# Kernel tuning notes

Hardware: AMD Instinct MI355X
Metric: run time of the kernel (lower is better)

The kernel has to match this reference:

```python
import jax, jax.numpy as jnp
import numpy as np

B, T, D, H, E = 32, 512, 768, 12, 6  # batch, seq(=input_size), n_embd, num_heads, per-head dim
DFF = 4 * D
EPS = 1e-5


def setup_inputs() -> dict:
    key = jax.random.key(0)
    ks = jax.random.split(key, 10)
    s = 0.02
    return {
        "x": jax.random.normal(ks[0], (B, T, D), jnp.float32),
        "Wq": jax.random.normal(ks[1], (H, D, E), jnp.float32) * s,
        "Wk": jax.random.normal(ks[2], (H, D, E), jnp.float32) * s,
        "Wv": jax.random.normal(ks[3], (H, D, E), jnp.float32) * s,
        "Wo": jax.random.normal(ks[4], (H * E, D), jnp.float32) * s,
        "bo": jnp.zeros((D,), jnp.float32),
        "W1": jax.random.normal(ks[5], (D, DFF), jnp.float32) * s,
        "b1": jnp.zeros((DFF,), jnp.float32),
        "W2": jax.random.normal(ks[6], (DFF, D), jnp.float32) * s,
        "b2": jnp.zeros((D,), jnp.float32),
        "g1": jnp.ones((D,), jnp.float32),
        "beta1": jnp.zeros((D,), jnp.float32),
        "g2": jnp.ones((D,), jnp.float32),
        "beta2": jnp.zeros((D,), jnp.float32),
    }


def _layernorm(x, g, b):
    m = jnp.mean(x, axis=-1, keepdims=True)
    v = jnp.var(x, axis=-1, keepdims=True)  # biased, matches torch LayerNorm
    return (x - m) * jax.lax.rsqrt(v + EPS) * g + b


def reference(x, Wq, Wk, Wv, Wo, bo, W1, b1, W2, b2, g1, beta1, g2, beta2):
    # --- pre-LN multi-head causal attention (dropout = identity, eval mode) ---
    xn = _layernorm(x, g1, beta1)
    q = jnp.einsum("btd,hde->bhte", xn, Wq)
    k = jnp.einsum("btd,hde->bhte", xn, Wk)
    v = jnp.einsum("btd,hde->bhte", xn, Wv)
    scores = jnp.einsum("bhte,bhse->bhts", q, k) * (E ** -0.5)
    causal = jnp.tril(jnp.ones((T, T), dtype=bool))
    scores = jnp.where(causal, scores, -jnp.inf)
    w = jax.nn.softmax(scores, axis=-1)
    o = jnp.einsum("bhts,bhse->bhte", w, v)
    o = o.transpose(0, 2, 1, 3).reshape(B, T, H * E)  # concat heads -> [B,T,72]
    x = x + o @ Wo + bo
    # --- pre-LN feed-forward ---
    y = _layernorm(x, g2, beta2)
    ff = jax.nn.relu(y @ W1 + b1) @ W2 + b2
    return x + ff
```

## Files before the change

kernel.cpp:

```cpp
#include <hip/hip_runtime.h>
#include <hip/hip_bf16.h>

#define BT 16384
#define DIM 768
#define NH 12
#define DFF 3072

typedef __attribute__((ext_vector_type(8))) short short8;
typedef __attribute__((ext_vector_type(4))) float floatx4;

using bf16 = __hip_bfloat16;

static __device__ __forceinline__ float b2f(bf16 v) { return __bfloat162float(v); }
static __device__ __forceinline__ bf16 f2b(float v) { return __float2bfloat16(v); }
static __device__ __forceinline__ void st_o(bf16* p, float v) { *p = __float2bfloat16(v); }
static __device__ __forceinline__ void st_o(float* p, float v) { *p = v; }

static __device__ __forceinline__ void gload_lds16(const void* g, void* l) {
    __builtin_amdgcn_global_load_lds(
        (const __attribute__((address_space(1))) unsigned int*)g,
        (__attribute__((address_space(3))) unsigned int*)l, 16, 0, 0);
}

__global__ __launch_bounds__(256) void pack_small_kernel(
    const float* __restrict__ Wq, const float* __restrict__ Wk, const float* __restrict__ Wv,
    const float* __restrict__ Wo, bf16* __restrict__ wqkv, bf16* __restrict__ wo_t)
{
    int i = blockIdx.x * 256 + threadIdx.x;
    const int S0 = 256 * 768, S1 = 768 * 96;
    if (i < S0) {
        int c = i / 768, dd = i % 768;
        float v = 0.f;
        if (c < 216) {
            int sel = c / 72, cc = c % 72, h = cc / 6, e = cc % 6;
            const float* W = (sel == 0) ? Wq : (sel == 1) ? Wk : Wv;
            v = W[((size_t)h * 768 + dd) * 6 + e];
        }
        wqkv[i] = f2b(v);
    } else if ((i -= S0) < S1) {
        int n = i / 96, r = i % 96;
        wo_t[i] = f2b(r < 72 ? Wo[r * 768 + n] : 0.f);
    }
}

__global__ __launch_bounds__(256) void transpose_kernel(
    const float* __restrict__ in, bf16* __restrict__ out, int R, int C)
{
    __shared__ float t[32][33];
    int c0 = blockIdx.x * 32, r0 = blockIdx.y * 32;
    int cx = threadIdx.x & 31, ry = threadIdx.x >> 5;
#pragma unroll
    for (int j = 0; j < 4; j++)
        t[ry + j * 8][cx] = in[(size_t)(r0 + ry + j * 8) * C + c0 + cx];
    __syncthreads();
    int rx = cx, cy = ry;
#pragma unroll
    for (int j = 0; j < 4; j++)
        out[(size_t)(c0 + cy + j * 8) * R + r0 + rx] = f2b(t[rx][cy + j * 8]);
}

__global__ __launch_bounds__(256) void ln_kernel(
    const float* __restrict__ x, const float* __restrict__ g, const float* __restrict__ be,
    bf16* __restrict__ out)
{
    int row = blockIdx.x;
    int tid = threadIdx.x;
    const float* xr = x + (size_t)row * DIM;
    float v[3], s = 0.f, s2 = 0.f;
#pragma unroll
    for (int i = 0; i < 3; i++) {
        float t = xr[tid + i * 256];
        v[i] = t; s += t; s2 += t * t;
    }
#pragma unroll
    for (int off = 32; off; off >>= 1) {
        s += __shfl_down(s, off);
        s2 += __shfl_down(s2, off);
    }
    __shared__ float red[8];
    int wv = tid >> 6, ln = tid & 63;
    if (ln == 0) { red[wv] = s; red[4 + wv] = s2; }
    __syncthreads();
    float ts = red[0] + red[1] + red[2] + red[3];
    float ts2 = red[4] + red[5] + red[6] + red[7];
    float mean = ts * (1.f / 768.f);
    float var = ts2 * (1.f / 768.f) - mean * mean;
    float rstd = rsqrtf(var + 1e-5f);
    bf16* orow = out + (size_t)row * DIM;
#pragma unroll
    for (int i = 0; i < 3; i++) {
        int dcol = tid + i * 256;
        orow[dcol] = f2b((v[i] - mean) * rstd * g[dcol] + be[dcol]);
    }
}

template <bool RELU, bool BIAS, bool RES, typename OutT>
__global__ __launch_bounds__(256) void gemm_kernel(
    const bf16* __restrict__ A, const bf16* __restrict__ Bt,
    const float* __restrict__ bias, const float* __restrict__ res,
    OutT* __restrict__ C, int M, int N, int K)
{
    __shared__ __align__(16) bf16 lA[128 * 32];
    __shared__ __align__(16) bf16 lB[128 * 32];
    const int tid = threadIdx.x;
    const int bm = blockIdx.x * 128;
    const int bn = blockIdx.y * 128;
    const int wave = tid >> 6, lane = tid & 63;
    const int wm = (wave >> 1) * 64, wn = (wave & 1) * 64;
    const int quad = lane >> 4, l16 = lane & 15;
    const int lrow = lane >> 2;
    const int lkc = (lane & 3) * 8;

    floatx4 acc[4][4] = {};

    for (int k0 = 0; k0 < K; k0 += 32) {
#pragma unroll
        for (int it = 0; it < 2; it++) {
            int r = wave * 32 + it * 16;
            gload_lds16(A + (size_t)(bm + r + lrow) * K + k0 + lkc, lA + r * 32);
            gload_lds16(Bt + (size_t)(bn + r + lrow) * K + k0 + lkc, lB + r * 32);
        }
        __syncthreads();
        short8 af[4], bfr[4];
#pragma unroll
        for (int mt = 0; mt < 4; mt++)
            af[mt] = *(const short8*)(lA + (wm + mt * 16 + l16) * 32 + quad * 8);
#pragma unroll
        for (int nt = 0; nt < 4; nt++)
            bfr[nt] = *(const short8*)(lB + (wn + nt * 16 + l16) * 32 + quad * 8);
#pragma unroll
        for (int mt = 0; mt < 4; mt++)
#pragma unroll
            for (int nt = 0; nt < 4; nt++)
                acc[mt][nt] = __builtin_amdgcn_mfma_f32_16x16x32_bf16(af[mt], bfr[nt], acc[mt][nt], 0, 0, 0);
        __syncthreads();
    }

#pragma unroll
    for (int mt = 0; mt < 4; mt++) {
#pragma unroll
        for (int nt = 0; nt < 4; nt++) {
            int gc = bn + wn + nt * 16 + l16;
            if (gc < N) {
#pragma unroll
                for (int r = 0; r < 4; r++) {
                    int gr = bm + wm + mt * 16 + quad * 4 + r;
                    float v0 = acc[mt][nt][r];
                    if constexpr (BIAS) v0 += bias[gc];
                    if constexpr (RES) v0 += res[(size_t)gr * N + gc];
                    if constexpr (RELU) v0 = fmaxf(v0, 0.f);
                    st_o(C + (size_t)gr * N + gc, v0);
                }
            }
        }
    }
}

__global__ __launch_bounds__(256) void attn_kernel(const bf16* __restrict__ qkv, bf16* __restrict__ o_pad)
{
    int blk = blockIdx.x;
    int half = blk & 1;
    int bh = blk >> 1;
    int b = bh / NH, h = bh % NH;
    int t0 = half * 256;
    int smax = t0 + 256;

    __shared__ float ks[512 * 6];
    __shared__ float vs[512 * 6];
    const bf16* base = qkv + (size_t)b * 512 * 216;
    for (int i = threadIdx.x; i < smax * 6; i += 256) {
        int s = i / 6, e = i % 6;
        ks[i] = b2f(base[s * 216 + 72 + h * 6 + e]);
        vs[i] = b2f(base[s * 216 + 144 + h * 6 + e]);
    }
    __syncthreads();

    int t = t0 + threadIdx.x;
    float q0 = b2f(base[t * 216 + h * 6 + 0]);
    float q1 = b2f(base[t * 216 + h * 6 + 1]);
    float q2 = b2f(base[t * 216 + h * 6 + 2]);
    float q3 = b2f(base[t * 216 + h * 6 + 3]);
    float q4 = b2f(base[t * 216 + h * 6 + 4]);
    float q5 = b2f(base[t * 216 + h * 6 + 5]);

    const float scale = 0.4082482904638630f;
    float m = -1e30f, l = 0.f;
    float o0 = 0, o1 = 0, o2 = 0, o3 = 0, o4 = 0, o5 = 0;
    for (int s = 0; s <= t; s++) {
        const float* kk = &ks[s * 6];
        float sc = (q0 * kk[0] + q1 * kk[1] + q2 * kk[2] + q3 * kk[3] + q4 * kk[4] + q5 * kk[5]) * scale;
        float nm = fmaxf(m, sc);
        float alpha = __expf(m - nm);
        float p = __expf(sc - nm);
        l = l * alpha + p;
        const float* vv = &vs[s * 6];
        o0 = o0 * alpha + p * vv[0];
        o1 = o1 * alpha + p * vv[1];
        o2 = o2 * alpha + p * vv[2];
        o3 = o3 * alpha + p * vv[3];
        o4 = o4 * alpha + p * vv[4];
        o5 = o5 * alpha + p * vv[5];
        m = nm;
    }
    float inv = 1.f / l;
    bf16* orow = o_pad + (size_t)(b * 512 + t) * 96 + h * 6;
    orow[0] = f2b(o0 * inv);
    orow[1] = f2b(o1 * inv);
    orow[2] = f2b(o2 * inv);
    orow[3] = f2b(o3 * inv);
    orow[4] = f2b(o4 * inv);
    orow[5] = f2b(o5 * inv);
}

extern "C" void kernel_launch(void* const* d_in, const int* in_sizes, int n_in,
                              void* d_out, int out_size, void* d_ws, size_t ws_size,
                              hipStream_t stream)
{
    const float* x   = (const float*)d_in[0];
    const float* Wq  = (const float*)d_in[1];
    const float* Wk  = (const float*)d_in[2];
    const float* Wv  = (const float*)d_in[3];
    const float* Wo  = (const float*)d_in[4];
    const float* bo  = (const float*)d_in[5];
    const float* W1  = (const float*)d_in[6];
    const float* b1  = (const float*)d_in[7];
    const float* W2  = (const float*)d_in[8];
    const float* b2  = (const float*)d_in[9];
    const float* g1  = (const float*)d_in[10];
    const float* be1 = (const float*)d_in[11];
    const float* g2  = (const float*)d_in[12];
    const float* be2 = (const float*)d_in[13];

    char* ws = (char*)d_ws;
    size_t off = 0;
    auto alloc = [&](size_t bytes) {
        void* p = ws + off;
        off = (off + bytes + 255) & ~(size_t)255;
        return p;
    };
    bf16*  xn    = (bf16*)alloc((size_t)BT * DIM * 2);
    bf16*  qkvb  = (bf16*)alloc((size_t)BT * 216 * 2);
    bf16*  o_pad = (bf16*)alloc((size_t)BT * 96 * 2);
    float* x1    = (float*)alloc((size_t)BT * DIM * 4);
    bf16*  ffb   = (bf16*)alloc((size_t)BT * DFF * 2);
    bf16*  wqkv  = (bf16*)alloc((size_t)256 * 768 * 2);
    bf16*  wo_t  = (bf16*)alloc((size_t)768 * 96 * 2);
    bf16*  w1t   = (bf16*)alloc((size_t)3072 * 768 * 2);
    bf16*  w2t   = (bf16*)alloc((size_t)768 * 3072 * 2);

    const int PACK_N = 256 * 768 + 768 * 96;
    pack_small_kernel<<<(PACK_N + 255) / 256, 256, 0, stream>>>(Wq, Wk, Wv, Wo, wqkv, wo_t);
    transpose_kernel<<<dim3(3072 / 32, 768 / 32), 256, 0, stream>>>(W1, w1t, 768, 3072);
    transpose_kernel<<<dim3(768 / 32, 3072 / 32), 256, 0, stream>>>(W2, w2t, 3072, 768);

    ln_kernel<<<BT, 256, 0, stream>>>(x, g1, be1, xn);
    gemm_kernel<false, false, false, bf16><<<dim3(128, 2), 256, 0, stream>>>(
        xn, wqkv, nullptr, nullptr, qkvb, BT, 216, 768);
    attn_kernel<<<32 * NH * 2, 256, 0, stream>>>(qkvb, o_pad);
    gemm_kernel<false, true, true, float><<<dim3(128, 6), 256, 0, stream>>>(
        o_pad, wo_t, bo, x, x1, BT, 768, 96);
    ln_kernel<<<BT, 256, 0, stream>>>(x1, g2, be2, xn);
    gemm_kernel<true, true, false, bf16><<<dim3(128, 24), 256, 0, stream>>>(
        xn, w1t, b1, nullptr, ffb, BT, 3072, 768);
    gemm_kernel<false, true, true, float><<<dim3(128, 6), 256, 0, stream>>>(
        ffb, w2t, b2, x1, (float*)d_out, BT, 768, 3072);
}
```

Before: 505.2 us.

## Vectorize layernorm, stage GEMM K in double slabs, LDS-staged bf16 epilogue, balance attention

Layernorm now uses 192 threads, each loading one float4 and writing four packed bf16 values, which cuts per-element memory instructions. The GEMM loads two 32-wide K slabs per barrier pair, halving synchronisations per K step. For bf16 outputs it stages the result tile in LDS and writes it back as coalesced 16-byte stores. Attention blocks now take interleaved 64-row query chunks, so the two halves of each causal head get similar work. The larger LDS footprint may lower GEMM occupancy.

```diff
diff --git a/kernel.cpp b/kernel.cpp
--- a/kernel.cpp
+++ b/kernel.cpp
@@ -8,13 +8,12 @@
 
 typedef __attribute__((ext_vector_type(8))) short short8;
 typedef __attribute__((ext_vector_type(4))) float floatx4;
+typedef __attribute__((ext_vector_type(4))) unsigned short ushort4b;
 
 using bf16 = __hip_bfloat16;
 
 static __device__ __forceinline__ float b2f(bf16 v) { return __bfloat162float(v); }
 static __device__ __forceinline__ bf16 f2b(float v) { return __float2bfloat16(v); }
-static __device__ __forceinline__ void st_o(bf16* p, float v) { *p = __float2bfloat16(v); }
-static __device__ __forceinline__ void st_o(float* p, float v) { *p = v; }
 
 static __device__ __forceinline__ void gload_lds16(const void* g, void* l) {
     __builtin_amdgcn_global_load_lds(
@@ -59,49 +58,53 @@
         out[(size_t)(c0 + cy + j * 8) * R + r0 + rx] = f2b(t[rx][cy + j * 8]);
 }
 
-__global__ __launch_bounds__(256) void ln_kernel(
+__global__ __launch_bounds__(192) void ln_kernel(
     const float* __restrict__ x, const float* __restrict__ g, const float* __restrict__ be,
     bf16* __restrict__ out)
 {
     int row = blockIdx.x;
     int tid = threadIdx.x;
-    const float* xr = x + (size_t)row * DIM;
-    float v[3], s = 0.f, s2 = 0.f;
-#pragma unroll
-    for (int i = 0; i < 3; i++) {
-        float t = xr[tid + i * 256];
-        v[i] = t; s += t; s2 += t * t;
-    }
+    const float4* xr = (const float4*)(x + (size_t)row * DIM);
+    float4 v = xr[tid];
+    float s = v.x + v.y + v.z + v.w;
+    float s2 = v.x * v.x + v.y * v.y + v.z * v.z + v.w * v.w;
 #pragma unroll
     for (int off = 32; off; off >>= 1) {
         s += __shfl_down(s, off);
         s2 += __shfl_down(s2, off);
     }
-    __shared__ float red[8];
+    __shared__ float red[6];
     int wv = tid >> 6, ln = tid & 63;
-    if (ln == 0) { red[wv] = s; red[4 + wv] = s2; }
+    if (ln == 0) { red[wv] = s; red[3 + wv] = s2; }
     __syncthreads();
-    float ts = red[0] + red[1] + red[2] + red[3];
-    float ts2 = red[4] + red[5] + red[6] + red[7];
+    float ts = red[0] + red[1] + red[2];
+    float ts2 = red[3] + red[4] + red[5];
     float mean = ts * (1.f / 768.f);
     float var = ts2 * (1.f / 768.f) - mean * mean;
     float rstd = rsqrtf(var + 1e-5f);
-    bf16* orow = out + (size_t)row * DIM;
-#pragma unroll
-    for (int i = 0; i < 3; i++) {
-        int dcol = tid + i * 256;
-        orow[dcol] = f2b((v[i] - mean) * rstd * g[dcol] + be[dcol]);
-    }
-}
-
-template <bool RELU, bool BIAS, bool RES, typename OutT>
+    int c = tid * 4;
+    float o0 = (v.x - mean) * rstd * g[c + 0] + be[c + 0];
+    float o1 = (v.y - mean) * rstd * g[c + 1] + be[c + 1];
+    float o2 = (v.z - mean) * rstd * g[c + 2] + be[c + 2];
+    float o3 = (v.w - mean) * rstd * g[c + 3] + be[c + 3];
+    bf16 h0 = f2b(o0), h1 = f2b(o1), h2 = f2b(o2), h3 = f2b(o3);
+    ushort4b pk;
+    pk[0] = *(unsigned short*)&h0; pk[1] = *(unsigned short*)&h1;
+    pk[2] = *(unsigned short*)&h2; pk[3] = *(unsigned short*)&h3;
+    *(ushort4b*)(out + (size_t)row * DIM + c) = pk;
+}
+
+template <int NSLAB, bool RELU, bool BIAS, bool RES, bool BF16OUT>
 __global__ __launch_bounds__(256) void gemm_kernel(
     const bf16* __restrict__ A, const bf16* __restrict__ Bt,
     const float* __restrict__ bias, const float* __restrict__ res,
-    OutT* __restrict__ C, int M, int N, int K)
-{
-    __shared__ __align__(16) bf16 lA[128 * 32];
-    __shared__ __align__(16) bf16 lB[128 * 32];
+    void* __restrict__ Cv, int M, int N, int K)
+{
+    constexpr int SMEM_BYTES = BF16OUT ? (128 * 136 * 2) : (NSLAB * 2 * 128 * 32 * 2);
+    __shared__ __align__(16) char smem[SMEM_BYTES];
+    bf16* lA = (bf16*)smem;
+    bf16* lB = lA + NSLAB * 128 * 32;
+
     const int tid = threadIdx.x;
     const int bm = blockIdx.x * 128;
     const int bn = blockIdx.y * 128;
@@ -113,43 +116,82 @@
 
     floatx4 acc[4][4] = {};
 
-    for (int k0 = 0; k0 < K; k0 += 32) {
-#pragma unroll
-        for (int it = 0; it < 2; it++) {
-            int r = wave * 32 + it * 16;
-            gload_lds16(A + (size_t)(bm + r + lrow) * K + k0 + lkc, lA + r * 32);
-            gload_lds16(Bt + (size_t)(bn + r + lrow) * K + k0 + lkc, lB + r * 32);
+    for (int k0 = 0; k0 < K; k0 += NSLAB * 32) {
+#pragma unroll
+        for (int s = 0; s < NSLAB; s++) {
+#pragma unroll
+            for (int it = 0; it < 2; it++) {
+                int r = wave * 32 + it * 16;
+                gload_lds16(A + (size_t)(bm + r + lrow) * K + k0 + s * 32 + lkc,
+                            lA + s * 4096 + r * 32);
+                gload_lds16(Bt + (size_t)(bn + r + lrow) * K + k0 + s * 32 + lkc,
+                            lB + s * 4096 + r * 32);
+            }
         }
         __syncthreads();
-        short8 af[4], bfr[4];
-#pragma unroll
-        for (int mt = 0; mt < 4; mt++)
-            af[mt] = *(const short8*)(lA + (wm + mt * 16 + l16) * 32 + quad * 8);
-#pragma unroll
-        for (int nt = 0; nt < 4; nt++)
-            bfr[nt] = *(const short8*)(lB + (wn + nt * 16 + l16) * 32 + quad * 8);
-#pragma unroll
-        for (int mt = 0; mt < 4; mt++)
+#pragma unroll
+        for (int s = 0; s < NSLAB; s++) {
+            short8 af[4], bfr[4];
+#pragma unroll
+            for (int mt = 0; mt < 4; mt++)
+                af[mt] = *(const short8*)(lA + s * 4096 + (wm + mt * 16 + l16) * 32 + quad * 8);
 #pragma unroll
             for (int nt = 0; nt < 4; nt++)
-                acc[mt][nt] = __builtin_amdgcn_mfma_f32_16x16x32_bf16(af[mt], bfr[nt], acc[mt][nt], 0, 0, 0);
+                bfr[nt] = *(const short8*)(lB + s * 4096 + (wn + nt * 16 + l16) * 32 + quad * 8);
+#pragma unroll
+            for (int mt = 0; mt < 4; mt++)
+#pragma unroll
+                for (int nt = 0; nt < 4; nt++)
+                    acc[mt][nt] = __builtin_amdgcn_mfma_f32_16x16x32_bf16(af[mt], bfr[nt], acc[mt][nt], 0, 0, 0);
+        }
         __syncthreads();
     }
 
-#pragma unroll
-    for (int mt = 0; mt < 4; mt++) {
-#pragma unroll
-        for (int nt = 0; nt < 4; nt++) {
-            int gc = bn + wn + nt * 16 + l16;
-            if (gc < N) {
+    if constexpr (BF16OUT) {
+        bf16* ltile = (bf16*)smem;
+#pragma unroll
+        for (int mt = 0; mt < 4; mt++) {
+#pragma unroll
+            for (int nt = 0; nt < 4; nt++) {
+                int tc = wn + nt * 16 + l16;
 #pragma unroll
                 for (int r = 0; r < 4; r++) {
-                    int gr = bm + wm + mt * 16 + quad * 4 + r;
+                    int tr = wm + mt * 16 + quad * 4 + r;
                     float v0 = acc[mt][nt][r];
-                    if constexpr (BIAS) v0 += bias[gc];
-                    if constexpr (RES) v0 += res[(size_t)gr * N + gc];
+                    if constexpr (BIAS) v0 += bias[bn + tc];
                     if constexpr (RELU) v0 = fmaxf(v0, 0.f);
-                    st_o(C + (size_t)gr * N + gc, v0);
+                    ltile[tr * 136 + tc] = f2b(v0);
+                }
+            }
+        }
+        __syncthreads();
+        bf16* C = (bf16*)Cv;
+        int rr0 = tid >> 4, col8 = (tid & 15) * 8;
+        int gc = bn + col8;
+#pragma unroll
+        for (int p = 0; p < 8; p++) {
+            int rr = p * 16 + rr0;
+            if (gc < N)
+                *(short8*)(C + (size_t)(bm + rr) * N + gc) =
+                    *(const short8*)(ltile + rr * 136 + col8);
+        }
+    } else {
+        float* C = (float*)Cv;
+#pragma unroll
+        for (int mt = 0; mt < 4; mt++) {
+#pragma unroll
+            for (int nt = 0; nt < 4; nt++) {
+                int gc = bn + wn + nt * 16 + l16;
+                if (gc < N) {
+#pragma unroll
+                    for (int r = 0; r < 4; r++) {
+                        int gr = bm + wm + mt * 16 + quad * 4 + r;
+                        float v0 = acc[mt][nt][r];
+                        if constexpr (BIAS) v0 += bias[gc];
+                        if constexpr (RES) v0 += res[(size_t)gr * N + gc];
+                        if constexpr (RELU) v0 = fmaxf(v0, 0.f);
+                        C[(size_t)gr * N + gc] = v0;
+                    }
                 }
             }
         }
@@ -162,8 +204,11 @@
     int half = blk & 1;
     int bh = blk >> 1;
     int b = bh / NH, h = bh % NH;
-    int t0 = half * 256;
-    int smax = t0 + 256;
+    int wave = threadIdx.x >> 6, lane = threadIdx.x & 63;
+    const int jmap0[4] = {0, 2, 5, 7}, jmap1[4] = {1, 3, 4, 6};
+    int j = half ? jmap1[wave] : jmap0[wave];
+    int t = j * 64 + lane;
+    int smax = half ? 448 : 512;
 
     __shared__ float ks[512 * 6];
     __shared__ float vs[512 * 6];
@@ -175,7 +220,6 @@
     }
     __syncthreads();
 
-    int t = t0 + threadIdx.x;
     float q0 = b2f(base[t * 216 + h * 6 + 0]);
     float q1 = b2f(base[t * 216 + h * 6 + 1]);
     float q2 = b2f(base[t * 216 + h * 6 + 2]);
@@ -253,15 +297,15 @@
     transpose_kernel<<<dim3(3072 / 32, 768 / 32), 256, 0, stream>>>(W1, w1t, 768, 3072);
     transpose_kernel<<<dim3(768 / 32, 3072 / 32), 256, 0, stream>>>(W2, w2t, 3072, 768);
 
-    ln_kernel<<<BT, 256, 0, stream>>>(x, g1, be1, xn);
-    gemm_kernel<false, false, false, bf16><<<dim3(128, 2), 256, 0, stream>>>(
+    ln_kernel<<<BT, 192, 0, stream>>>(x, g1, be1, xn);
+    gemm_kernel<2, false, false, false, true><<<dim3(128, 2), 256, 0, stream>>>(
         xn, wqkv, nullptr, nullptr, qkvb, BT, 216, 768);
     attn_kernel<<<32 * NH * 2, 256, 0, stream>>>(qkvb, o_pad);
-    gemm_kernel<false, true, true, float><<<dim3(128, 6), 256, 0, stream>>>(
+    gemm_kernel<1, false, true, true, false><<<dim3(128, 6), 256, 0, stream>>>(
         o_pad, wo_t, bo, x, x1, BT, 768, 96);
-    ln_kernel<<<BT, 256, 0, stream>>>(x1, g2, be2, xn);
-    gemm_kernel<true, true, false, bf16><<<dim3(128, 24), 256, 0, stream>>>(
+    ln_kernel<<<BT, 192, 0, stream>>>(x1, g2, be2, xn);
+    gemm_kernel<2, true, true, false, true><<<dim3(128, 24), 256, 0, stream>>>(
         xn, w1t, b1, nullptr, ffb, BT, 3072, 768);
-    gemm_kernel<false, true, true, float><<<dim3(128, 6), 256, 0, stream>>>(
+    gemm_kernel<2, false, true, true, false><<<dim3(128, 6), 256, 0, stream>>>(
         ffb, w2t, b2, x1, (float*)d_out, BT, 768, 3072);
 }
```

Measured after the change: 458.1 us. -9.3%, faster.
